# Kernel tuning notes

Measured on AMD Instinct MI355X. Metric: run time of the kernel, lower is better.

The kernel has to match this reference:

```python
import jax, jax.numpy as jnp
import numpy as np

CUTOFF = 5.0
LOG2 = float(np.log(2.0))

def ssp(x):
    # shifted softplus: softplus(x) - log(2)
    return jax.nn.softplus(x) - LOG2

def setup_inputs() -> dict:
    key = jax.random.key(0)
    ks = jax.random.split(key, 12)
    Nb, Na, Nnbh = 8, 1024, 64
    A, F, S = 128, 128, 50
    x = jax.random.normal(ks[0], (Nb, Na, A), dtype=jnp.float32)
    r_ij = jax.random.uniform(ks[1], (Nb, Na, Nnbh), dtype=jnp.float32) * 8.0  # some beyond cutoff=5
    neighbors = jax.random.randint(ks[2], (Nb, Na, Nnbh), 0, Na)
    neighbor_mask = (jax.random.uniform(ks[3], (Nb, Na, Nnbh)) > 0.1).astype(jnp.float32)
    f_ij = jax.random.normal(ks[4], (Nb, Na, Nnbh, S), dtype=jnp.float32)
    sc = lambda n: 1.0 / np.sqrt(n)
    W_in2f = jax.random.normal(ks[5], (F, A), dtype=jnp.float32) * sc(A)
    W_f1 = jax.random.normal(ks[6], (F, S), dtype=jnp.float32) * sc(S)
    b_f1 = jnp.zeros((F,), jnp.float32)
    W_f2 = jax.random.normal(ks[7], (F, F), dtype=jnp.float32) * sc(F)
    b_f2 = jnp.zeros((F,), jnp.float32)
    W_f2out = jax.random.normal(ks[8], (A, F), dtype=jnp.float32) * sc(F)
    b_f2out = jnp.zeros((A,), jnp.float32)
    W_dense = jax.random.normal(ks[9], (A, A), dtype=jnp.float32) * sc(A)
    b_dense = jnp.zeros((A,), jnp.float32)
    return {"x": x, "r_ij": r_ij, "neighbors": neighbors, "neighbor_mask": neighbor_mask,
            "f_ij": f_ij, "W_in2f": W_in2f, "W_f1": W_f1, "b_f1": b_f1, "W_f2": W_f2,
            "b_f2": b_f2, "W_f2out": W_f2out, "b_f2out": b_f2out, "W_dense": W_dense,
            "b_dense": b_dense}

def reference(x, r_ij, neighbors, neighbor_mask, f_ij, W_in2f, W_f1, b_f1, W_f2, b_f2,
              W_f2out, b_f2out, W_dense, b_dense):
    # filter network: Dense(S->F, ssp) -> Dense(F->F)
    W = ssp(jnp.einsum('bans,fs->banf', f_ij, W_f1) + b_f1)
    W = jnp.einsum('bang,fg->banf', W, W_f2) + b_f2          # [Nb,Na,Nnbh,F]
    # hard cutoff
    C = (r_ij <= CUTOFF).astype(W.dtype)                      # [Nb,Na,Nnbh]
    W = W * C[..., None]
    # in2f (no bias)
    y = jnp.einsum('bai,fi->baf', x, W_in2f)                  # [Nb,Na,F]
    # gather neighbor features along atom axis
    yg = jax.vmap(lambda yb, nb: yb[nb])(y, neighbors)        # [Nb,Na,Nnbh,F]
    # masked sum over neighbor axis (Aggregate, mean=False)
    v = jnp.sum(yg * W * neighbor_mask[..., None], axis=2)    # [Nb,Na,F]
    # f2out: Dense(F->A) with ssp, then dense: Dense(A->A)
    v = ssp(jnp.einsum('baf,af->ba' + 'f'[0:0] + 'a'[0:0], v, W_f2out).reshape(v.shape[:2] + (W_f2out.shape[0],)) if False else ssp(v @ W_f2out.T + b_f2out))
    out = v @ W_dense.T + b_dense                             # [Nb,Na,A]
    return out
```

## Files before the change

kernel.cpp:

```cpp
#include <hip/hip_runtime.h>
#include <math.h>


#define RCUT  5.0f
#define LOG2F_ 0.69314718055994530942f
#define LOG2E_ 1.44269504088896340736f

typedef __bf16 bf16x8_t __attribute__((ext_vector_type(8)));
typedef float  f32x4_t  __attribute__((ext_vector_type(4)));

static __device__ __forceinline__ float sspf(float x) {
    float e  = exp2f(-LOG2E_ * fabsf(x));
    float lg = log2f(1.0f + e);
    return fmaf(lg, LOG2F_, fmaxf(x, 0.0f) - LOG2F_);
}
static __device__ __forceinline__ unsigned pack2h(__bf16 a, __bf16 b) {
    union { __bf16 h[2]; unsigned u; } un; un.h[0] = a; un.h[1] = b; return un.u;
}
static __device__ __forceinline__ unsigned pack2f(float a, float b) {
    return pack2h((__bf16)a, (__bf16)b);
}

__global__ __launch_bounds__(256) void prep_kernel(
    const float* __restrict__ W1, const float* __restrict__ W2,
    const float* __restrict__ Wb,
    const float* __restrict__ Wc,
    const float* __restrict__ Wf,
    unsigned* __restrict__ prep)
{
    int i = blockIdx.x * 256 + threadIdx.x;
    if (i < 4096) {
        int sw = i >> 10, ft = (i >> 9) & 1, kh = (i >> 8) & 1;
        int sl = (i >> 2) & 63, j = i & 3;
        int sq = sl >> 4, sm = sl & 15;
        int f = 32 * sw + 16 * ft + sm;
        int c = kh * 16 + 4 * sq + j;
        int k0 = 2 * c, k1 = 2 * c + 1;
        float a = (k0 < 50) ? W1[f * 50 + k0] : 0.0f;
        float b = (k1 < 50) ? W1[f * 50 + k1] : 0.0f;
        prep[i] = pack2f(a, b);
    } else if (i < 12288) {
        int s = i - 4096;
        int sw = s >> 11, ft = (s >> 10) & 1, kq = (s >> 8) & 3;
        int sl = (s >> 2) & 63, j = s & 3;
        int sq = sl >> 4, sm = sl & 15;
        int f = 32 * sw + 16 * ft + sm;
        int c = 16 * kq + 4 * sq + j;
        float2 wv = ((const float2*)W2)[f * 64 + c];
        prep[i] = pack2f(wv.x, wv.y);
    } else {
        int s = i - 12288;
        int L = s >> 14;
        int r = s & 16383;
        int hl = r >> 13;
        int e = r & 8191;
        int sw = e >> 11, ft = (e >> 10) & 1, kq = (e >> 8) & 3;
        int sl = (e >> 2) & 63, j = e & 3;
        int sq = sl >> 4, sm = sl & 15;
        int f = 32 * sw + 16 * ft + sm;
        int c = 16 * kq + 4 * sq + j;
        const float* src = (L == 0) ? Wb : (L == 1) ? Wc : Wf;
        float2 wv = ((const float2*)src)[f * 64 + c];
        if (hl == 0) {
            prep[i] = pack2h((__bf16)wv.x, (__bf16)wv.y);
        } else {
            __bf16 h0 = (__bf16)wv.x, h1 = (__bf16)wv.y;
            prep[i] = pack2f(wv.x - (float)h0, wv.y - (float)h1);
        }
    }
}

__global__ __launch_bounds__(256, 4) void k1_kernel(
    const float* __restrict__ x,
    const unsigned* __restrict__ Wh, const unsigned* __restrict__ Wl,
    float* __restrict__ yout)
{
    __shared__ __bf16 Ah[16 * 136];
    __shared__ __bf16 Al[16 * 136];

    const int t = threadIdx.x;
    const int atom0 = (blockIdx.x >> 1) * 16;
    const int fh = blockIdx.x & 1;
    const int w = t >> 6, l = t & 63, m = l & 15, q = l >> 4;

    {
        const float4* A4 = (const float4*)(x + (size_t)atom0 * 128);
        unsigned* AhU = (unsigned*)Ah;
        unsigned* AlU = (unsigned*)Al;
        #pragma unroll
        for (int r = 0; r < 2; ++r) {
            int lin4 = r * 256 + t;
            int a = lin4 >> 5, k4 = lin4 & 31;
            float4 xv = A4[lin4];
            __bf16 h0=(__bf16)xv.x, h1=(__bf16)xv.y, h2=(__bf16)xv.z, h3=(__bf16)xv.w;
            int idx = a * 68 + 2 * k4;
            AhU[idx]     = pack2h(h0, h1);
            AhU[idx + 1] = pack2h(h2, h3);
            AlU[idx]     = pack2f(xv.x - (float)h0, xv.y - (float)h1);
            AlU[idx + 1] = pack2f(xv.z - (float)h2, xv.w - (float)h3);
        }
    }
    __syncthreads();

    const int ftile = fh * 4 + w;
    const int f = 16 * ftile + m;
    f32x4_t acc = {0.f, 0.f, 0.f, 0.f};
    #pragma unroll
    for (int kk = 0; kk < 4; ++kk) {
        int off = m * 136 + 32 * kk + 8 * q;
        bf16x8_t ah = *(const bf16x8_t*)&Ah[off];
        bf16x8_t al = *(const bf16x8_t*)&Al[off];
        int wo = (ftile * 4 + kk) * 256 + l * 4;
        bf16x8_t wh = *(const bf16x8_t*)(Wh + wo);
        bf16x8_t wl = *(const bf16x8_t*)(Wl + wo);
        acc = __builtin_amdgcn_mfma_f32_16x16x32_bf16(ah, wh, acc, 0, 0, 0);
        acc = __builtin_amdgcn_mfma_f32_16x16x32_bf16(ah, wl, acc, 0, 0, 0);
        acc = __builtin_amdgcn_mfma_f32_16x16x32_bf16(al, wh, acc, 0, 0, 0);
    }
    #pragma unroll
    for (int r = 0; r < 4; ++r)
        yout[(size_t)(atom0 + 4 * q + r) * 128 + f] = acc[r];
}

__global__ __launch_bounds__(256, 4) void interaction_kernel(
    const float* __restrict__ rij, const int* __restrict__ nbrs,
    const float* __restrict__ mask, const float* __restrict__ fij,
    const float* __restrict__ b1, const float* __restrict__ b2,
    const unsigned* __restrict__ W1S,
    const unsigned* __restrict__ W2S,
    const float* __restrict__ y, float* __restrict__ v)
{
    __shared__ __bf16 Hh[64 * 136];
    __shared__ __bf16 Hl[64 * 136];
    __shared__ float  cb[64];
    __shared__ int    nb[64];

    const int t  = threadIdx.x;
    const int a  = blockIdx.x;
    const int bi = a >> 10;
    const int p0 = a * 64;
    const int w = t >> 6, l = t & 63, m = l & 15, q = l >> 4;

    if (t < 64) {
        float r = rij[p0 + t];
        cb[t] = (r <= RCUT) ? mask[p0 + t] : 0.0f;
        nb[t] = (bi << 10) + nbrs[p0 + t];
    }

    {
        const float* frow = fij + (size_t)(p0 + 16 * w + m) * 50;
        float kv[16];
        #pragma unroll
        for (int j2 = 0; j2 < 4; ++j2) {
            float2 xv = *(const float2*)(frow + 8 * q + 2 * j2);
            kv[2 * j2] = xv.x; kv[2 * j2 + 1] = xv.y;
        }
        #pragma unroll
        for (int j2 = 0; j2 < 4; ++j2) {
            int k = 32 + 8 * q + 2 * j2;
            float2 xv = make_float2(0.f, 0.f);
            if (k < 50) xv = *(const float2*)(frow + k);
            kv[8 + 2 * j2] = xv.x; kv[9 + 2 * j2] = xv.y;
        }
        union { __bf16 h[16]; bf16x8_t v8[2]; } uh, ul;
        #pragma unroll
        for (int k = 0; k < 16; ++k) {
            __bf16 hi = (__bf16)kv[k];
            uh.h[k] = hi;
            ul.h[k] = (__bf16)(kv[k] - (float)hi);
        }
        #pragma unroll 2
        for (int ftile = 0; ftile < 8; ++ftile) {
            float bb = b1[16 * ftile + m];
            f32x4_t acc = {bb, bb, bb, bb};
            bf16x8_t w0 = *(const bf16x8_t*)(W1S + (ftile * 2 + 0) * 256 + l * 4);
            bf16x8_t w1 = *(const bf16x8_t*)(W1S + (ftile * 2 + 1) * 256 + l * 4);
            acc = __builtin_amdgcn_mfma_f32_16x16x32_bf16(uh.v8[0], w0, acc, 0, 0, 0);
            acc = __builtin_amdgcn_mfma_f32_16x16x32_bf16(ul.v8[0], w0, acc, 0, 0, 0);
            acc = __builtin_amdgcn_mfma_f32_16x16x32_bf16(uh.v8[1], w1, acc, 0, 0, 0);
            acc = __builtin_amdgcn_mfma_f32_16x16x32_bf16(ul.v8[1], w1, acc, 0, 0, 0);
            #pragma unroll
            for (int r = 0; r < 4; ++r) {
                int n = 16 * w + 4 * q + r;
                float hv = sspf(acc[r]);
                __bf16 hh = (__bf16)hv;
                Hh[n * 136 + 16 * ftile + m] = hh;
                Hl[n * 136 + 16 * ftile + m] = (__bf16)(hv - (float)hh);
            }
        }
    }
    __syncthreads();

    const int f0 = 32 * w + m;
    const int f1 = f0 + 16;
    const float bb2_0 = b2[f0], bb2_1 = b2[f1];
    bf16x8_t w2f0[4], w2f1[4];
    #pragma unroll
    for (int kq = 0; kq < 4; ++kq) {
        w2f0[kq] = *(const bf16x8_t*)(W2S + ((w * 2 + 0) * 4 + kq) * 256 + l * 4);
        w2f1[kq] = *(const bf16x8_t*)(W2S + ((w * 2 + 1) * 4 + kq) * 256 + l * 4);
    }
    float pv0 = 0.0f, pv1 = 0.0f;
    #pragma unroll 1
    for (int mt = 0; mt < 4; ++mt) {
        f32x4_t acc0 = {bb2_0, bb2_0, bb2_0, bb2_0};
        f32x4_t acc1 = {bb2_1, bb2_1, bb2_1, bb2_1};
        #pragma unroll
        for (int kq = 0; kq < 4; ++kq) {
            int hoff = (16 * mt + m) * 136 + 32 * kq + 8 * q;
            bf16x8_t hh = *(const bf16x8_t*)&Hh[hoff];
            bf16x8_t hl = *(const bf16x8_t*)&Hl[hoff];
            acc0 = __builtin_amdgcn_mfma_f32_16x16x32_bf16(hh, w2f0[kq], acc0, 0, 0, 0);
            acc0 = __builtin_amdgcn_mfma_f32_16x16x32_bf16(hl, w2f0[kq], acc0, 0, 0, 0);
            acc1 = __builtin_amdgcn_mfma_f32_16x16x32_bf16(hh, w2f1[kq], acc1, 0, 0, 0);
            acc1 = __builtin_amdgcn_mfma_f32_16x16x32_bf16(hl, w2f1[kq], acc1, 0, 0, 0);
        }
        #pragma unroll
        for (int r = 0; r < 4; ++r) {
            int n = 16 * mt + 4 * q + r;
            float cn = cb[n];
            const float* yrow = y + (size_t)nb[n] * 128;
            pv0 = fmaf(cn * yrow[f0], acc0[r], pv0);
            pv1 = fmaf(cn * yrow[f1], acc1[r], pv1);
        }
    }
    pv0 += __shfl_xor(pv0, 16);
    pv0 += __shfl_xor(pv0, 32);
    pv1 += __shfl_xor(pv1, 16);
    pv1 += __shfl_xor(pv1, 32);
    if (l < 16) {
        v[(size_t)a * 128 + f0] = pv0;
        v[(size_t)a * 128 + f1] = pv1;
    }
}

__global__ __launch_bounds__(256, 4) void mgemm2_kernel(
    const float* A,
    const unsigned* __restrict__ W1h, const unsigned* __restrict__ W1l,
    const float* __restrict__ bias1, int nssp1,
    const unsigned* __restrict__ W2h, const unsigned* __restrict__ W2l,
    const float* __restrict__ bias2, int nssp2,
    float* C)
{
    extern __shared__ float smf[];
    __bf16* Ah = (__bf16*)smf;
    __bf16* Al = (__bf16*)(smf + 1088);
    unsigned* AhU = (unsigned*)Ah;
    unsigned* AlU = (unsigned*)Al;

    const int t = threadIdx.x;
    const int atom0 = blockIdx.x * 16;
    const int w = t >> 6, l = t & 63, m = l & 15, q = l >> 4;

    {
        const float4* A4 = (const float4*)(A + (size_t)atom0 * 128);
        #pragma unroll
        for (int r = 0; r < 2; ++r) {
            int lin4 = r * 256 + t;
            int a = lin4 >> 5, k4 = lin4 & 31;
            float4 xv = A4[lin4];
            __bf16 h0=(__bf16)xv.x, h1=(__bf16)xv.y, h2=(__bf16)xv.z, h3=(__bf16)xv.w;
            int idx = a * 68 + 2 * k4;
            AhU[idx]     = pack2h(h0, h1);
            AhU[idx + 1] = pack2h(h2, h3);
            AlU[idx]     = pack2f(xv.x - (float)h0, xv.y - (float)h1);
            AlU[idx + 1] = pack2f(xv.z - (float)h2, xv.w - (float)h3);
        }
    }
    __syncthreads();

    bf16x8_t ah[4], al[4];
    #pragma unroll
    for (int kk = 0; kk < 4; ++kk) {
        int off = m * 136 + 32 * kk + 8 * q;
        ah[kk] = *(const bf16x8_t*)&Ah[off];
        al[kk] = *(const bf16x8_t*)&Al[off];
    }
    f32x4_t acc[2];
    int fidx[2];
    #pragma unroll
    for (int ft = 0; ft < 2; ++ft) {
        fidx[ft] = 16 * (2 * w + ft) + m;
        float b = bias1 ? bias1[fidx[ft]] : 0.0f;
        acc[ft] = (f32x4_t){b, b, b, b};
    }
    #pragma unroll
    for (int ft = 0; ft < 2; ++ft) {
        #pragma unroll
        for (int kk = 0; kk < 4; ++kk) {
            int wo = ((2 * w + ft) * 4 + kk) * 256 + l * 4;
            bf16x8_t wh = *(const bf16x8_t*)(W1h + wo);
            bf16x8_t wl = *(const bf16x8_t*)(W1l + wo);
            acc[ft] = __builtin_amdgcn_mfma_f32_16x16x32_bf16(ah[kk], wh, acc[ft], 0, 0, 0);
            acc[ft] = __builtin_amdgcn_mfma_f32_16x16x32_bf16(ah[kk], wl, acc[ft], 0, 0, 0);
            acc[ft] = __builtin_amdgcn_mfma_f32_16x16x32_bf16(al[kk], wh, acc[ft], 0, 0, 0);
        }
    }
    #pragma unroll
    for (int ft = 0; ft < 2; ++ft)
        #pragma unroll
        for (int r = 0; r < 4; ++r) {
            float o = acc[ft][r];
            if (nssp1 >= 1) o = sspf(o);
            if (nssp1 >= 2) o = sspf(o);
            acc[ft][r] = o;
        }

    __syncthreads();
    #pragma unroll
    for (int ft = 0; ft < 2; ++ft)
        #pragma unroll
        for (int r = 0; r < 4; ++r) {
            float o = acc[ft][r];
            __bf16 hh = (__bf16)o;
            Ah[(4 * q + r) * 136 + fidx[ft]] = hh;
            Al[(4 * q + r) * 136 + fidx[ft]] = (__bf16)(o - (float)hh);
        }
    __syncthreads();

    #pragma unroll
    for (int kk = 0; kk < 4; ++kk) {
        int off = m * 136 + 32 * kk + 8 * q;
        ah[kk] = *(const bf16x8_t*)&Ah[off];
        al[kk] = *(const bf16x8_t*)&Al[off];
    }
    #pragma unroll
    for (int ft = 0; ft < 2; ++ft) {
        float b = bias2 ? bias2[fidx[ft]] : 0.0f;
        acc[ft] = (f32x4_t){b, b, b, b};
    }
    #pragma unroll
    for (int ft = 0; ft < 2; ++ft) {
        #pragma unroll
        for (int kk = 0; kk < 4; ++kk) {
            int wo = ((2 * w + ft) * 4 + kk) * 256 + l * 4;
            bf16x8_t wh = *(const bf16x8_t*)(W2h + wo);
            bf16x8_t wl = *(const bf16x8_t*)(W2l + wo);
            acc[ft] = __builtin_amdgcn_mfma_f32_16x16x32_bf16(ah[kk], wh, acc[ft], 0, 0, 0);
            acc[ft] = __builtin_amdgcn_mfma_f32_16x16x32_bf16(ah[kk], wl, acc[ft], 0, 0, 0);
            acc[ft] = __builtin_amdgcn_mfma_f32_16x16x32_bf16(al[kk], wh, acc[ft], 0, 0, 0);
        }
    }
    #pragma unroll
    for (int ft = 0; ft < 2; ++ft)
        #pragma unroll
        for (int r = 0; r < 4; ++r) {
            float o = acc[ft][r];
            if (nssp2 >= 1) o = sspf(o);
            if (nssp2 >= 2) o = sspf(o);
            C[(size_t)(atom0 + 4 * q + r) * 128 + fidx[ft]] = o;
        }
}

extern "C" void kernel_launch(void* const* d_in, const int* in_sizes, int n_in,
                              void* d_out, int out_size, void* d_ws, size_t ws_size,
                              hipStream_t stream) {
    const float* x        = (const float*)d_in[0];
    const float* rij      = (const float*)d_in[1];
    const int*   nbrs     = (const int*)  d_in[2];
    const float* mask     = (const float*)d_in[3];
    const float* fij      = (const float*)d_in[4];
    const float* W_in2f   = (const float*)d_in[5];
    const float* W_f1     = (const float*)d_in[6];
    const float* b_f1     = (const float*)d_in[7];
    const float* W_f2     = (const float*)d_in[8];
    const float* b_f2     = (const float*)d_in[9];
    const float* W_f2out  = (const float*)d_in[10];
    const float* b_f2out  = (const float*)d_in[11];
    const float* W_dense  = (const float*)d_in[12];
    const float* b_dense  = (const float*)d_in[13];
    float* out = (float*)d_out;

    float*    y    = (float*)d_ws;
    unsigned* prep = (unsigned*)((char*)d_ws + (4u << 20));
    const unsigned* W1S    = prep;
    const unsigned* W2S    = prep + 4096;
    const unsigned* f2o_h  = prep + 12288, *f2o_l  = prep + 20480;
    const unsigned* den_h  = prep + 28672, *den_l  = prep + 36864;
    const unsigned* in2f_h = prep + 45056, *in2f_l = prep + 53248;

    const int MG2_LDS = 2176 * 4;

    prep_kernel<<<240, 256, 0, stream>>>(W_f1, W_f2, W_f2out, W_dense, W_in2f, prep);
    k1_kernel<<<1024, 256, 0, stream>>>(x, in2f_h, in2f_l, y);
    interaction_kernel<<<8192, 256, 0, stream>>>(
        rij, nbrs, mask, fij, b_f1, b_f2, W1S, W2S, y, out);
    mgemm2_kernel<<<512, 256, MG2_LDS, stream>>>(
        out, f2o_h, f2o_l, b_f2out, 2, den_h, den_l, b_dense, 0, out);
}
```

Measured before the change: 256.0 us.

## Prefetch gathered neighbor features into registers and split MFMA accumulator chains

Each thread now loads its neighbors' cutoff/mask values, indices and gathered y features into registers at kernel start, instead of staging them in shared memory and gathering y after the filter GEMMs. The intent is to overlap the latency of the irregular global gather with the first filter-network GEMM. The hi/lo bf16 MFMA pairs now accumulate into separate accumulators that are summed afterwards, which breaks the serial dependency between consecutive MFMAs. The second GEMM loop is fully unrolled. These changes raise register pressure (32 extra floats plus doubled accumulators), which could reduce occupancy under the 256-thread, 4-block launch bound.

```diff
diff --git a/kernel.cpp b/kernel.cpp
--- a/kernel.cpp
+++ b/kernel.cpp
@@ -132,19 +132,26 @@
 {
     __shared__ __bf16 Hh[64 * 136];
     __shared__ __bf16 Hl[64 * 136];
-    __shared__ float  cb[64];
-    __shared__ int    nb[64];
 
     const int t  = threadIdx.x;
     const int a  = blockIdx.x;
     const int bi = a >> 10;
     const int p0 = a * 64;
     const int w = t >> 6, l = t & 63, m = l & 15, q = l >> 4;
-
-    if (t < 64) {
-        float r = rij[p0 + t];
-        cb[t] = (r <= RCUT) ? mask[p0 + t] : 0.0f;
-        nb[t] = (bi << 10) + nbrs[p0 + t];
+    const int f0 = 32 * w + m;
+    const int f1 = f0 + 16;
+
+    float cy0[16], cy1[16];
+    #pragma unroll
+    for (int i = 0; i < 16; ++i) {
+        int mt = i >> 2, r = i & 3;
+        int n = 16 * mt + 4 * q + r;
+        float rr = rij[p0 + n];
+        float cn = (rr <= RCUT) ? mask[p0 + n] : 0.0f;
+        int nbv = (bi << 10) + nbrs[p0 + n];
+        const float* yrow = y + (size_t)nbv * 128;
+        cy0[i] = cn * yrow[f0];
+        cy1[i] = cn * yrow[f1];
     }
 
     {
@@ -172,17 +179,18 @@
         #pragma unroll 2
         for (int ftile = 0; ftile < 8; ++ftile) {
             float bb = b1[16 * ftile + m];
-            f32x4_t acc = {bb, bb, bb, bb};
+            f32x4_t acch = {bb, bb, bb, bb};
+            f32x4_t accl = {0.f, 0.f, 0.f, 0.f};
             bf16x8_t w0 = *(const bf16x8_t*)(W1S + (ftile * 2 + 0) * 256 + l * 4);
             bf16x8_t w1 = *(const bf16x8_t*)(W1S + (ftile * 2 + 1) * 256 + l * 4);
-            acc = __builtin_amdgcn_mfma_f32_16x16x32_bf16(uh.v8[0], w0, acc, 0, 0, 0);
-            acc = __builtin_amdgcn_mfma_f32_16x16x32_bf16(ul.v8[0], w0, acc, 0, 0, 0);
-            acc = __builtin_amdgcn_mfma_f32_16x16x32_bf16(uh.v8[1], w1, acc, 0, 0, 0);
-            acc = __builtin_amdgcn_mfma_f32_16x16x32_bf16(ul.v8[1], w1, acc, 0, 0, 0);
+            acch = __builtin_amdgcn_mfma_f32_16x16x32_bf16(uh.v8[0], w0, acch, 0, 0, 0);
+            accl = __builtin_amdgcn_mfma_f32_16x16x32_bf16(ul.v8[0], w0, accl, 0, 0, 0);
+            acch = __builtin_amdgcn_mfma_f32_16x16x32_bf16(uh.v8[1], w1, acch, 0, 0, 0);
+            accl = __builtin_amdgcn_mfma_f32_16x16x32_bf16(ul.v8[1], w1, accl, 0, 0, 0);
             #pragma unroll
             for (int r = 0; r < 4; ++r) {
                 int n = 16 * w + 4 * q + r;
-                float hv = sspf(acc[r]);
+                float hv = sspf(acch[r] + accl[r]);
                 __bf16 hh = (__bf16)hv;
                 Hh[n * 136 + 16 * ftile + m] = hh;
                 Hl[n * 136 + 16 * ftile + m] = (__bf16)(hv - (float)hh);
@@ -191,8 +199,6 @@
     }
     __syncthreads();
 
-    const int f0 = 32 * w + m;
-    const int f1 = f0 + 16;
     const float bb2_0 = b2[f0], bb2_1 = b2[f1];
     bf16x8_t w2f0[4], w2f1[4];
     #pragma unroll
@@ -201,27 +207,28 @@
         w2f1[kq] = *(const bf16x8_t*)(W2S + ((w * 2 + 1) * 4 + kq) * 256 + l * 4);
     }
     float pv0 = 0.0f, pv1 = 0.0f;
-    #pragma unroll 1
+    #pragma unroll
     for (int mt = 0; mt < 4; ++mt) {
-        f32x4_t acc0 = {bb2_0, bb2_0, bb2_0, bb2_0};
-        f32x4_t acc1 = {bb2_1, bb2_1, bb2_1, bb2_1};
+        f32x4_t a0h = {bb2_0, bb2_0, bb2_0, bb2_0};
+        f32x4_t a0l = {0.f, 0.f, 0.f, 0.f};
+        f32x4_t a1h = {bb2_1, bb2_1, bb2_1, bb2_1};
+        f32x4_t a1l = {0.f, 0.f, 0.f, 0.f};
         #pragma unroll
         for (int kq = 0; kq < 4; ++kq) {
             int hoff = (16 * mt + m) * 136 + 32 * kq + 8 * q;
             bf16x8_t hh = *(const bf16x8_t*)&Hh[hoff];
             bf16x8_t hl = *(const bf16x8_t*)&Hl[hoff];
-            acc0 = __builtin_amdgcn_mfma_f32_16x16x32_bf16(hh, w2f0[kq], acc0, 0, 0, 0);
-            acc0 = __builtin_amdgcn_mfma_f32_16x16x32_bf16(hl, w2f0[kq], acc0, 0, 0, 0);
-            acc1 = __builtin_amdgcn_mfma_f32_16x16x32_bf16(hh, w2f1[kq], acc1, 0, 0, 0);
-            acc1 = __builtin_amdgcn_mfma_f32_16x16x32_bf16(hl, w2f1[kq], acc1, 0, 0, 0);
+            a0h = __builtin_amdgcn_mfma_f32_16x16x32_bf16(hh, w2f0[kq], a0h, 0, 0, 0);
+            a0l = __builtin_amdgcn_mfma_f32_16x16x32_bf16(hl, w2f0[kq], a0l, 0, 0, 0);
+            a1h = __builtin_amdgcn_mfma_f32_16x16x32_bf16(hh, w2f1[kq], a1h, 0, 0, 0);
+            a1l = __builtin_amdgcn_mfma_f32_16x16x32_bf16(hl, w2f1[kq], a1l, 0, 0, 0);
         }
         #pragma unroll
         for (int r = 0; r < 4; ++r) {
-            int n = 16 * mt + 4 * q + r;
-            float cn = cb[n];
-            const float* yrow = y + (size_t)nb[n] * 128;
-            pv0 = fmaf(cn * yrow[f0], acc0[r], pv0);
-            pv1 = fmaf(cn * yrow[f1], acc1[r], pv1);
+            float s0 = a0h[r] + a0l[r];
+            float s1 = a1h[r] + a1l[r];
+            pv0 = fmaf(cy0[mt * 4 + r], s0, pv0);
+            pv1 = fmaf(cy1[mt * 4 + r], s1, pv1);
         }
     }
     pv0 += __shfl_xor(pv0, 16);
```

Result: slower. 283.9 us (+10.9%).
